# Performance work log

Hardware: AMD Instinct MI355X
Metric: run time of the kernel (lower is better)

The kernel has to match this reference:

```python
import jax, jax.numpy as jnp
import numpy as np

N = 50000          # num member nodes == num provider nodes
E = 800000         # provider->member bipartite edges (avg degree 16)
IN_M = 128; IN_P = 128; HID = 128; HEADS = 4; LAT = 64
NEG = 0.2          # leaky_relu negative slope (PyG GATConv default)


def gat_conv(x, src, dst, W, a_src, a_dst, b, heads, ch):
    """PyG-style GATConv (eval mode, concat heads). x:[N,F], src/dst:[Etot]."""
    n = x.shape[0]
    h = (x @ W).reshape(n, heads, ch)                       # [N,H,C]
    s = jnp.sum(h * a_src, axis=-1)                         # [N,H]
    d = jnp.sum(h * a_dst, axis=-1)                         # [N,H]
    e = jax.nn.leaky_relu(s[src] + d[dst], NEG)             # [Etot,H]
    # segment softmax over edges grouped by destination node
    m = jax.ops.segment_max(e, dst, num_segments=n)
    p = jnp.exp(e - m[dst])
    z = jax.ops.segment_sum(p, dst, num_segments=n)
    alpha = p / (z[dst] + 1e-16)                            # [Etot,H]
    out = jax.ops.segment_sum(h[src] * alpha[..., None], dst, num_segments=n)
    return out.reshape(n, heads * ch) + b


def setup_inputs() -> dict:
    key = jax.random.key(0)
    ks = jax.random.split(key, 24)
    gl = lambda k, shape, fan: (jax.random.normal(k, shape, jnp.float32) / np.sqrt(fan).astype(np.float32))
    return {
        "x_member": jax.random.normal(ks[0], (N, IN_M), jnp.float32),
        "x_provider": jax.random.normal(ks[1], (N, IN_P), jnp.float32),
        "edge_index": jax.random.randint(ks[2], (2, E), 0, N),
        "W1_m": gl(ks[3], (IN_M, HID), IN_M),
        "a_src1_m": gl(ks[4], (HEADS, HID // HEADS), HID // HEADS),
        "a_dst1_m": gl(ks[5], (HEADS, HID // HEADS), HID // HEADS),
        "b1_m": jnp.zeros((HID,), jnp.float32),
        "W2_m": gl(ks[6], (HID, LAT), HID),
        "a_src2_m": gl(ks[7], (1, LAT), LAT),
        "a_dst2_m": gl(ks[8], (1, LAT), LAT),
        "b2_m": jnp.zeros((LAT,), jnp.float32),
        "W1_p": gl(ks[9], (IN_P, HID), IN_P),
        "a_src1_p": gl(ks[10], (HEADS, HID // HEADS), HID // HEADS),
        "a_dst1_p": gl(ks[11], (HEADS, HID // HEADS), HID // HEADS),
        "b1_p": jnp.zeros((HID,), jnp.float32),
        "W2_p": gl(ks[12], (HID, LAT), HID),
        "a_src2_p": gl(ks[13], (1, LAT), LAT),
        "a_dst2_p": gl(ks[14], (1, LAT), LAT),
        "b2_p": jnp.zeros((LAT,), jnp.float32),
        "Wd_m": gl(ks[15], (LAT, IN_M), LAT),
        "bd_m": jnp.zeros((IN_M,), jnp.float32),
        "Wd_p": gl(ks[16], (LAT, IN_P), LAT),
        "bd_p": jnp.zeros((IN_P,), jnp.float32),
    }


def reference(x_member, x_provider, edge_index,
              W1_m, a_src1_m, a_dst1_m, b1_m, W2_m, a_src2_m, a_dst2_m, b2_m,
              W1_p, a_src1_p, a_dst1_p, b1_p, W2_p, a_src2_p, a_dst2_p, b2_p,
              Wd_m, bd_m, Wd_p, bd_p):
    prov, memb = edge_index[0], edge_index[1]
    loop = jnp.arange(N)
    # member graph: self loops + (provider -> member); provider graph: reverse
    m_src = jnp.concatenate([loop, prov]); m_dst = jnp.concatenate([loop, memb])
    p_src = jnp.concatenate([loop, memb]); p_dst = jnp.concatenate([loop, prov])

    xm = jax.nn.elu(gat_conv(x_member, m_src, m_dst, W1_m, a_src1_m, a_dst1_m, b1_m, HEADS, HID // HEADS))
    z_m = gat_conv(xm, m_src, m_dst, W2_m, a_src2_m, a_dst2_m, b2_m, 1, LAT)

    xp = jax.nn.elu(gat_conv(x_provider, p_src, p_dst, W1_p, a_src1_p, a_dst1_p, b1_p, HEADS, HID // HEADS))
    z_p = gat_conv(xp, p_src, p_dst, W2_p, a_src2_p, a_dst2_p, b2_p, 1, LAT)

    x_hat_member = z_m @ Wd_m + bd_m
    x_hat_provider = z_p @ Wd_p + bd_p
    edge_logits = jnp.sum(z_p[prov] * z_m[memb], axis=1)
    return (x_hat_member, x_hat_provider, edge_logits)
```

## Files before the change

### kernel.cpp

```cpp
#include <hip/hip_runtime.h>
#include <hip/hip_fp16.h>
#include <stdint.h>

__device__ __forceinline__ unsigned int pack_h2(float a, float b) {
    return (unsigned int)__half_as_ushort(__float2half(a)) |
           ((unsigned int)__half_as_ushort(__float2half(b)) << 16);
}
__device__ __forceinline__ float4 cvt_h4(uint2 r) {
    __half2 h0 = *reinterpret_cast<__half2*>(&r.x);
    __half2 h1 = *reinterpret_cast<__half2*>(&r.y);
    float2 f0 = __half22float2(h0), f1 = __half22float2(h1);
    return make_float4(f0.x, f0.y, f1.x, f1.y);
}

template<int K, int COUT, bool ADD_BIAS, bool IN_HALF, bool OUT_HALF, int SDH>
__global__ __launch_bounds__(256) void gemm_kernel(const void* __restrict__ X0,
                                                   const void* __restrict__ X1,
                                                   const float* __restrict__ W0,
                                                   const float* __restrict__ W1,
                                                   const float* __restrict__ b0,
                                                   const float* __restrict__ b1,
                                                   const float* __restrict__ as0,
                                                   const float* __restrict__ ad0,
                                                   const float* __restrict__ as1,
                                                   const float* __restrict__ ad1,
                                                   float* __restrict__ s_out,
                                                   float* __restrict__ d_out,
                                                   void* __restrict__ out0,
                                                   void* __restrict__ out1, int n)
{
    constexpr int KC   = 64;
    constexpr int CPT  = (COUT >= 128) ? 8 : 4;
    constexpr int TX   = COUT / CPT;
    constexpr int TY   = 256 / TX;
    constexpr int ROWS = TY * 4;

    __shared__ float Wl[KC * COUT];
    __shared__ float Xl[KC * ROWS];

    const int side = blockIdx.y;
    const void*  Xv   = side ? X1 : X0;
    const float* W    = side ? W1 : W0;
    const float* bias = side ? b1 : b0;
    void* outp        = side ? out1 : out0;

    const int tid  = threadIdx.x;
    const int row0 = blockIdx.x * ROWS;
    const int tx = tid % TX, ty = tid / TX;
    const int c0 = tx * CPT;

    float acc[4][CPT];
    #pragma unroll
    for (int i = 0; i < 4; ++i)
        #pragma unroll
        for (int j = 0; j < CPT; ++j) acc[i][j] = 0.f;

    for (int k0 = 0; k0 < K; k0 += KC) {
        for (int i = tid; i < KC * COUT / 4; i += 256) {
            int e0 = i * 4;
            int r = e0 / COUT, c = e0 - r * COUT;
            reinterpret_cast<float4*>(Wl)[i] =
                *reinterpret_cast<const float4*>(W + (size_t)(k0 + r) * COUT + c);
        }
        for (int i = tid; i < ROWS * KC / 4; i += 256) {
            int r = i / (KC / 4), c4 = i - r * (KC / 4);
            int gr = row0 + r;
            float4 v = make_float4(0.f, 0.f, 0.f, 0.f);
            if (gr < n) {
                if constexpr (IN_HALF) {
                    const __half* X = (const __half*)Xv;
                    v = cvt_h4(*reinterpret_cast<const uint2*>(X + (size_t)gr * K + k0 + c4 * 4));
                } else {
                    const float* X = (const float*)Xv;
                    v = *reinterpret_cast<const float4*>(X + (size_t)gr * K + k0 + c4 * 4);
                }
            }
            int cb = c4 * 4;
            Xl[(cb + 0) * ROWS + r] = v.x;
            Xl[(cb + 1) * ROWS + r] = v.y;
            Xl[(cb + 2) * ROWS + r] = v.z;
            Xl[(cb + 3) * ROWS + r] = v.w;
        }
        __syncthreads();

        #pragma unroll 16
        for (int kk = 0; kk < KC; ++kk) {
            float b[CPT];
            #pragma unroll
            for (int j = 0; j < CPT; ++j) b[j] = Wl[kk * COUT + c0 + j];
            float4 a4 = *reinterpret_cast<const float4*>(Xl + kk * ROWS + ty * 4);
            float a[4] = {a4.x, a4.y, a4.z, a4.w};
            #pragma unroll
            for (int i = 0; i < 4; ++i)
                #pragma unroll
                for (int j = 0; j < CPT; ++j)
                    acc[i][j] = fmaf(a[i], b[j], acc[i][j]);
        }
        __syncthreads();
    }

    float ascr[CPT], adtr[CPT];
    int hd = 0;
    if constexpr (SDH > 0) {
        constexpr int CHh = COUT / SDH;
        hd = c0 / CHh;
        const float* asc = (side ? as1 : as0) + c0;
        const float* adt = (side ? ad1 : ad0) + c0;
        #pragma unroll
        for (int j = 0; j < CPT; ++j) { ascr[j] = asc[j]; adtr[j] = adt[j]; }
    }

    #pragma unroll
    for (int i = 0; i < 4; ++i) {
        int gr = row0 + ty * 4 + i;
        if (gr < n) {
            float v[CPT];
            #pragma unroll
            for (int j = 0; j < CPT; ++j) {
                v[j] = acc[i][j];
                if constexpr (ADD_BIAS) v[j] += bias[c0 + j];
            }
            if constexpr (SDH > 0) {
                constexpr int CHh = COUT / SDH;
                constexpr int GL = CHh / CPT;
                float ps = 0.f, pd = 0.f;
                #pragma unroll
                for (int j = 0; j < CPT; ++j) {
                    ps = fmaf(v[j], ascr[j], ps);
                    pd = fmaf(v[j], adtr[j], pd);
                }
                #pragma unroll
                for (int o = 1; o < GL; o <<= 1) {
                    ps += __shfl_xor(ps, o, 64);
                    pd += __shfl_xor(pd, o, 64);
                }
                if ((tx % GL) == 0) {
                    size_t gi = (size_t)(side ? n + gr : gr) * SDH + hd;
                    s_out[gi] = ps; d_out[gi] = pd;
                }
            }
            if constexpr (OUT_HALF) {
                __half* po = (__half*)outp + (size_t)gr * COUT + c0;
                if constexpr (CPT == 8) {
                    uint4 w;
                    w.x = pack_h2(v[0], v[1]); w.y = pack_h2(v[2], v[3]);
                    w.z = pack_h2(v[4], v[5]); w.w = pack_h2(v[6], v[7]);
                    *reinterpret_cast<uint4*>(po) = w;
                } else {
                    uint2 w;
                    w.x = pack_h2(v[0], v[1]); w.y = pack_h2(v[2], v[3]);
                    *reinterpret_cast<uint2*>(po) = w;
                }
            } else {
                float* po = (float*)outp + (size_t)gr * COUT + c0;
                #pragma unroll
                for (int j = 0; j < CPT; ++j) po[j] = v[j];
            }
        }
    }
}

#define BSH 7
#define BCAP 2560
#define CHUNK_E 4096

__global__ __launch_bounds__(256) void bucket_scatter_kernel(const int* __restrict__ prov,
                                                             const int* __restrict__ memb,
                                                             int* __restrict__ bcnt,
                                                             int2* __restrict__ bstore,
                                                             int e, int n, int nbuck)
{
    __shared__ int hist[1024];
    __shared__ int lbase[1024];
    const int tid = threadIdx.x;
    const int e0 = blockIdx.x * CHUNK_E;
    const int e1 = min(e, e0 + CHUNK_E);

    for (int i = tid; i < nbuck; i += 256) hist[i] = 0;
    __syncthreads();
    for (int t = e0 + tid; t < e1; t += 256) {
        int m = memb[t], p = prov[t];
        atomicAdd(&hist[m >> BSH], 1);
        atomicAdd(&hist[(n + p) >> BSH], 1);
    }
    __syncthreads();
    for (int i = tid; i < nbuck; i += 256) {
        int h = hist[i];
        lbase[i] = (h > 0) ? atomicAdd(&bcnt[i], h) : 0;
        hist[i] = 0;
    }
    __syncthreads();
    for (int t = e0 + tid; t < e1; t += 256) {
        int m = memb[t], p = prov[t];
        int b1 = m >> BSH;
        int pos1 = lbase[b1] + atomicAdd(&hist[b1], 1);
        if (pos1 < BCAP) bstore[(size_t)b1 * BCAP + pos1] = make_int2(m, p);
        int d2 = n + p;
        int b2 = d2 >> BSH;
        int pos2 = lbase[b2] + atomicAdd(&hist[b2], 1);
        if (pos2 < BCAP) bstore[(size_t)b2 * BCAP + pos2] = make_int2(d2, m);
    }
}

__global__ __launch_bounds__(1024) void bucket_scan_kernel(const int* __restrict__ bcnt,
                                                           int* __restrict__ bbase,
                                                           int* __restrict__ roff,
                                                           int nb, int n2)
{
    __shared__ int tmp[1024];
    int tid = threadIdx.x;
    int v = (tid < nb) ? min(bcnt[tid], BCAP) : 0;
    tmp[tid] = v; __syncthreads();
    for (int o = 1; o < 1024; o <<= 1) {
        int x = (tid >= o) ? tmp[tid - o] : 0;
        __syncthreads();
        tmp[tid] += x;
        __syncthreads();
    }
    bbase[tid] = tmp[tid] - v;
    if (tid == 0) roff[n2] = tmp[1023];
}

__global__ __launch_bounds__(256) void bucket_build_kernel(const int* __restrict__ bcnt,
                                                           const int* __restrict__ bbase,
                                                           const int2* __restrict__ bstore,
                                                           int* __restrict__ roff,
                                                           int* __restrict__ colA,
                                                           int n2)
{
    __shared__ int2 ent[BCAP];
    __shared__ int  colL[BCAP];
    __shared__ int  cnts[128], pref[128], curs[128];

    const int b = blockIdx.x, tid = threadIdx.x;
    const int node0 = b << BSH;
    const int cnt  = min(bcnt[b], BCAP);
    const int base = bbase[b];

    if (tid < 128) cnts[tid] = 0;
    __syncthreads();
    for (int i = tid; i < cnt; i += 256) {
        int2 v = bstore[(size_t)b * BCAP + i];
        ent[i] = v;
        atomicAdd(&cnts[v.x - node0], 1);
    }
    __syncthreads();
    if (tid < 128) pref[tid] = cnts[tid];
    __syncthreads();
    #pragma unroll
    for (int o = 1; o < 128; o <<= 1) {
        int x = 0;
        if (tid < 128 && tid >= o) x = pref[tid - o];
        __syncthreads();
        if (tid < 128) pref[tid] += x;
        __syncthreads();
    }
    if (tid < 128) {
        int node = node0 + tid;
        if (node < n2) roff[node] = base + pref[tid] - cnts[tid];
        curs[tid] = 0;
    }
    __syncthreads();
    for (int i = tid; i < cnt; i += 256) {
        int2 v = ent[i];
        int loc = v.x - node0;
        int slot = (pref[loc] - cnts[loc]) + atomicAdd(&curs[loc], 1);
        colL[slot] = v.y;
    }
    __syncthreads();
    for (int i = tid; i < cnt; i += 256) colA[base + i] = colL[i];
}

template<int H>
__device__ __forceinline__ float selH(const float* arr, int hd) {
    float v = arr[0];
    #pragma unroll
    for (int hh = 1; hh < H; ++hh) v = (hd == hh) ? arr[hh] : v;
    return v;
}

template<int C, int H, bool ELU, bool OUTH>
__device__ __forceinline__ void agg_one_fullwave(int iG, int lN, int lane,
                                                 const __half* __restrict__ hf,
                                                 const float* __restrict__ sarr,
                                                 const float* __restrict__ sb,
                                                 const float* __restrict__ darr,
                                                 const int* __restrict__ roff,
                                                 const int* __restrict__ col,
                                                 const float* __restrict__ bias,
                                                 void* __restrict__ out,
                                                 float* alsW, int* srcsW)
{
    constexpr int CH = C / H;
    constexpr int LR = C / 4;
    constexpr int EP = 64 / LR;
    const int start = roff[iG], end = roff[iG + 1];
    const int deg = end - start;

    float dh[H], es[H];
    #pragma unroll
    for (int hh = 0; hh < H; ++hh) dh[hh] = darr[(size_t)iG * H + hh];
    #pragma unroll
    for (int hh = 0; hh < H; ++hh) {
        float e = sarr[(size_t)iG * H + hh] + dh[hh];
        es[hh] = fmaxf(e, 0.2f * e);
    }

    if (deg <= 64) {
        int srcL = (lane < deg) ? col[start + lane] : 0;
        float pl[H], zh[H];
        if (lane < deg) {
            #pragma unroll
            for (int hh = 0; hh < H; ++hh) {
                float e = sb[(size_t)srcL * H + hh] + dh[hh];
                pl[hh] = __expf(fmaxf(e, 0.2f * e));
            }
        } else {
            #pragma unroll
            for (int hh = 0; hh < H; ++hh) pl[hh] = 0.f;
        }
        #pragma unroll
        for (int hh = 0; hh < H; ++hh) zh[hh] = pl[hh];
        #pragma unroll
        for (int hh = 0; hh < H; ++hh)
            for (int o = 32; o >= 1; o >>= 1)
                zh[hh] += __shfl_xor(zh[hh], o, 64);
        if (lane < deg) srcsW[lane] = srcL;
        float aself[H];
        #pragma unroll
        for (int hh = 0; hh < H; ++hh) {
            float se = __expf(es[hh]);
            float invz = 1.f / (zh[hh] + se + 1e-16f);
            aself[hh] = se * invz;
            if (lane < deg) alsW[hh * 65 + lane] = pl[hh] * invz;
        }
        asm volatile("s_waitcnt lgkmcnt(0)" ::: "memory");

        const int sub = lane / LR;
        const int q   = lane % LR;
        const int c0  = q * 4;
        const int hd  = c0 / CH;

        float4 acc = make_float4(0.f, 0.f, 0.f, 0.f);
        if (sub == 0) {
            float4 hv = cvt_h4(*reinterpret_cast<const uint2*>(hf + (size_t)lN * C + c0));
            float a = selH<H>(aself, hd);
            acc.x = a * hv.x; acc.y = a * hv.y; acc.z = a * hv.z; acc.w = a * hv.w;
        }
        const float* alsB = alsW + hd * 65;
        int t = sub;
#define GSTEP(U)                                                                     \
        while (t + (U - 1) * EP < deg) {                                             \
            int ss[U]; float aa[U]; uint2 rr[U];                                     \
            _Pragma("unroll")                                                        \
            for (int u = 0; u < U; ++u) { ss[u] = srcsW[t + u * EP]; aa[u] = alsB[t + u * EP]; } \
            _Pragma("unroll")                                                        \
            for (int u = 0; u < U; ++u)                                              \
                rr[u] = *reinterpret_cast<const uint2*>(hf + (size_t)ss[u] * C + c0); \
            _Pragma("unroll")                                                        \
            for (int u = 0; u < U; ++u) {                                            \
                float4 hv = cvt_h4(rr[u]);                                           \
                acc.x = fmaf(aa[u], hv.x, acc.x);                                    \
                acc.y = fmaf(aa[u], hv.y, acc.y);                                    \
                acc.z = fmaf(aa[u], hv.z, acc.z);                                    \
                acc.w = fmaf(aa[u], hv.w, acc.w);                                    \
            }                                                                        \
            t += U * EP;                                                             \
        }
        GSTEP(8)
        GSTEP(4)
        GSTEP(2)
        GSTEP(1)
#undef GSTEP
        #pragma unroll
        for (int o = LR; o < 64; o <<= 1) {
            acc.x += __shfl_xor(acc.x, o, 64);
            acc.y += __shfl_xor(acc.y, o, 64);
            acc.z += __shfl_xor(acc.z, o, 64);
            acc.w += __shfl_xor(acc.w, o, 64);
        }
        if (sub == 0) {
            float4 bv = *reinterpret_cast<const float4*>(bias + c0);
            float4 v = make_float4(acc.x + bv.x, acc.y + bv.y, acc.z + bv.z, acc.w + bv.w);
            if constexpr (ELU) {
                v.x = (v.x > 0.f) ? v.x : (__expf(v.x) - 1.f);
                v.y = (v.y > 0.f) ? v.y : (__expf(v.y) - 1.f);
                v.z = (v.z > 0.f) ? v.z : (__expf(v.z) - 1.f);
                v.w = (v.w > 0.f) ? v.w : (__expf(v.w) - 1.f);
            }
            if constexpr (OUTH) {
                uint2 w; w.x = pack_h2(v.x, v.y); w.y = pack_h2(v.z, v.w);
                *reinterpret_cast<uint2*>((__half*)out + (size_t)lN * C + c0) = w;
            } else {
                *reinterpret_cast<float4*>((float*)out + (size_t)lN * C + c0) = v;
            }
        }
        return;
    }

    float zh[H];
    #pragma unroll
    for (int hh = 0; hh < H; ++hh) zh[hh] = 0.f;
    for (int base = start; base < end; base += 64) {
        int idx = base + lane;
        if (idx < end) {
            int src = col[idx];
            #pragma unroll
            for (int hh = 0; hh < H; ++hh) {
                float e = sb[(size_t)src * H + hh] + dh[hh];
                e = fmaxf(e, 0.2f * e);
                zh[hh] += __expf(e);
            }
        }
    }
    #pragma unroll
    for (int hh = 0; hh < H; ++hh) {
        for (int o = 32; o >= 1; o >>= 1) zh[hh] += __shfl_xor(zh[hh], o, 64);
        zh[hh] += __expf(es[hh]);
    }

    constexpr int CPL = C / 64;
    const int cc0 = lane * CPL;
    const int hdl = cc0 / CH;
    const float invz = 1.f / (zh[hdl] + 1e-16f);
    const float d_l  = dh[hdl];

    float acc2[CPL];
    {
        float aself = __expf(es[hdl]) * invz;
        #pragma unroll
        for (int j = 0; j < CPL; ++j) acc2[j] = aself * __half2float(hf[(size_t)lN * C + cc0 + j]);
    }
    for (int base = start; base < end; base += 64) {
        int idx = base + lane;
        int srcL2 = (idx < end) ? col[idx] : 0;
        int cnt2 = min(64, end - base);
        for (int t = 0; t < cnt2; ++t) {
            int st = __shfl(srcL2, t, 64);
            float e = sb[(size_t)st * H + hdl] + d_l;
            e = fmaxf(e, 0.2f * e);
            float a = __expf(e) * invz;
            #pragma unroll
            for (int j = 0; j < CPL; ++j)
                acc2[j] = fmaf(a, __half2float(hf[(size_t)st * C + cc0 + j]), acc2[j]);
        }
    }
    #pragma unroll
    for (int j = 0; j < CPL; ++j) {
        int c = cc0 + j;
        float v = acc2[j] + bias[c];
        if constexpr (ELU) v = (v > 0.f) ? v : (__expf(v) - 1.f);
        if constexpr (OUTH) ((__half*)out)[(size_t)lN * C + c] = __float2half(v);
        else                ((float*)out)[(size_t)lN * C + c] = v;
    }
}

template<int C, int H, bool ELU, bool OUTH>
__global__ __launch_bounds__(256) void agg_kernel(const __half* __restrict__ hm,
                                                  const __half* __restrict__ hp,
                                                  const float* __restrict__ sarr,
                                                  const float* __restrict__ darr,
                                                  const int* __restrict__ roff,
                                                  const int* __restrict__ col,
                                                  const float* __restrict__ bias_m,
                                                  const float* __restrict__ bias_p,
                                                  void* __restrict__ out_m,
                                                  void* __restrict__ out_p, int N)
{
    constexpr int CH  = C / H;
    constexpr int LRd = C / 8;
    constexpr int EPd = 32 / LRd;
    constexpr int H33 = H * 33;
    constexpr int ALSZ = (2 * H33 > H * 65) ? 2 * H33 : H * 65;
    __shared__ float als[4][ALSZ];
    __shared__ int   srcs[4][64];

    const int n2 = 2 * N;
    const int wslot = threadIdx.x >> 6;
    const int wv    = (blockIdx.x * 256 + threadIdx.x) >> 6;
    const int lane  = threadIdx.x & 63;
    const int g = lane >> 5, l = lane & 31;
    const int i0 = wv * 2;
    if (i0 >= n2) return;

    const bool nval = (i0 + g) < n2;
    const int iN = nval ? (i0 + g) : (n2 - 1);
    const int side = (iN >= N) ? 1 : 0;
    const int lN = iN - side * N;
    const __half* hf = side ? hp : hm;
    const float* sb = sarr + (size_t)side * N * H;
    const float* biasS = side ? bias_p : bias_m;
    void* outS = side ? out_p : out_m;

    const int start = roff[iN], end = roff[iN + 1];
    const int deg = nval ? (end - start) : 0;
    const int degO = __shfl_xor(deg, 32, 64);
    const int degm = max(deg, degO);

    if (degm <= 32) {
        float dh[H], es[H];
        if constexpr (H == 4) {
            float4 dv = *reinterpret_cast<const float4*>(darr + (size_t)iN * 4);
            float4 sv = *reinterpret_cast<const float4*>(sarr + (size_t)iN * 4);
            dh[0] = dv.x; dh[1] = dv.y; dh[2] = dv.z; dh[3] = dv.w;
            float ev[4] = {sv.x + dv.x, sv.y + dv.y, sv.z + dv.z, sv.w + dv.w};
            #pragma unroll
            for (int hh = 0; hh < 4; ++hh) es[hh] = fmaxf(ev[hh], 0.2f * ev[hh]);
        } else {
            #pragma unroll
            for (int hh = 0; hh < H; ++hh) {
                dh[hh] = darr[(size_t)iN * H + hh];
                float e = sarr[(size_t)iN * H + hh] + dh[hh];
                es[hh] = fmaxf(e, 0.2f * e);
            }
        }

        int srcL = (l < deg) ? col[start + l] : 0;
        float pl[H];
        if (l < deg) {
            if constexpr (H == 4) {
                float4 sv = *reinterpret_cast<const float4*>(sb + (size_t)srcL * 4);
                float ee[4] = {sv.x + dh[0], sv.y + dh[1], sv.z + dh[2], sv.w + dh[3]};
                #pragma unroll
                for (int hh = 0; hh < 4; ++hh) pl[hh] = __expf(fmaxf(ee[hh], 0.2f * ee[hh]));
            } else {
                #pragma unroll
                for (int hh = 0; hh < H; ++hh) {
                    float e = sb[(size_t)srcL * H + hh] + dh[hh];
                    pl[hh] = __expf(fmaxf(e, 0.2f * e));
                }
            }
        } else {
            #pragma unroll
            for (int hh = 0; hh < H; ++hh) pl[hh] = 0.f;
        }
        float zh[H];
        #pragma unroll
        for (int hh = 0; hh < H; ++hh) zh[hh] = pl[hh];
        #pragma unroll
        for (int hh = 0; hh < H; ++hh)
            #pragma unroll
            for (int o = 16; o >= 1; o >>= 1)
                zh[hh] += __shfl_xor(zh[hh], o, 64);
        if (l < deg) srcs[wslot][g * 32 + l] = srcL;
        float aself[H];
        #pragma unroll
        for (int hh = 0; hh < H; ++hh) {
            float se = __expf(es[hh]);
            float invz = 1.f / (zh[hh] + se + 1e-16f);
            aself[hh] = se * invz;
            if (l < deg) als[wslot][g * H33 + hh * 33 + l] = pl[hh] * invz;
        }
        asm volatile("s_waitcnt lgkmcnt(0)" ::: "memory");

        const int sub = l / LRd;
        const int q   = l % LRd;
        const int c0  = q * 8;
        const int hd  = c0 / CH;

        float acc[8];
        #pragma unroll
        for (int j = 0; j < 8; ++j) acc[j] = 0.f;
        if (sub == 0) {
            uint4 r = *reinterpret_cast<const uint4*>(hf + (size_t)lN * C + c0);
            float4 lo = cvt_h4(make_uint2(r.x, r.y));
            float4 hi = cvt_h4(make_uint2(r.z, r.w));
            float a = selH<H>(aself, hd);
            acc[0] = a * lo.x; acc[1] = a * lo.y; acc[2] = a * lo.z; acc[3] = a * lo.w;
            acc[4] = a * hi.x; acc[5] = a * hi.y; acc[6] = a * hi.z; acc[7] = a * hi.w;
        }
        const int*   srcB = &srcs[wslot][g * 32];
        const float* alsB = &als[wslot][g * H33 + hd * 33];
        int t = sub;
#define GSTEP(U)                                                                     \
        while (t + (U - 1) * EPd < deg) {                                            \
            int ss[U]; float aa[U]; uint4 rr[U];                                     \
            _Pragma("unroll")                                                        \
            for (int u = 0; u < U; ++u) { ss[u] = srcB[t + u * EPd]; aa[u] = alsB[t + u * EPd]; } \
            _Pragma("unroll")                                                        \
            for (int u = 0; u < U; ++u)                                              \
                rr[u] = *reinterpret_cast<const uint4*>(hf + (size_t)ss[u] * C + c0); \
            _Pragma("unroll")                                                        \
            for (int u = 0; u < U; ++u) {                                            \
                float4 lo = cvt_h4(make_uint2(rr[u].x, rr[u].y));                    \
                float4 hi = cvt_h4(make_uint2(rr[u].z, rr[u].w));                    \
                acc[0] = fmaf(aa[u], lo.x, acc[0]);                                  \
                acc[1] = fmaf(aa[u], lo.y, acc[1]);                                  \
                acc[2] = fmaf(aa[u], lo.z, acc[2]);                                  \
                acc[3] = fmaf(aa[u], lo.w, acc[3]);                                  \
                acc[4] = fmaf(aa[u], hi.x, acc[4]);                                  \
                acc[5] = fmaf(aa[u], hi.y, acc[5]);                                  \
                acc[6] = fmaf(aa[u], hi.z, acc[6]);                                  \
                acc[7] = fmaf(aa[u], hi.w, acc[7]);                                  \
            }                                                                        \
            t += U * EPd;                                                            \
        }
        GSTEP(8)
        GSTEP(4)
        GSTEP(2)
        GSTEP(1)
#undef GSTEP
        #pragma unroll
        for (int o = LRd; o < 32; o <<= 1) {
            #pragma unroll
            for (int j = 0; j < 8; ++j) acc[j] += __shfl_xor(acc[j], o, 64);
        }
        if (sub == 0 && nval) {
            float4 b0 = *reinterpret_cast<const float4*>(biasS + c0);
            float4 b1 = *reinterpret_cast<const float4*>(biasS + c0 + 4);
            float v[8] = {acc[0] + b0.x, acc[1] + b0.y, acc[2] + b0.z, acc[3] + b0.w,
                          acc[4] + b1.x, acc[5] + b1.y, acc[6] + b1.z, acc[7] + b1.w};
            if constexpr (ELU) {
                #pragma unroll
                for (int j = 0; j < 8; ++j) v[j] = (v[j] > 0.f) ? v[j] : (__expf(v[j]) - 1.f);
            }
            if constexpr (OUTH) {
                uint4 w;
                w.x = pack_h2(v[0], v[1]); w.y = pack_h2(v[2], v[3]);
                w.z = pack_h2(v[4], v[5]); w.w = pack_h2(v[6], v[7]);
                *reinterpret_cast<uint4*>((__half*)outS + (size_t)lN * C + c0) = w;
            } else {
                float* po = (float*)outS + (size_t)lN * C + c0;
                *reinterpret_cast<float4*>(po)     = make_float4(v[0], v[1], v[2], v[3]);
                *reinterpret_cast<float4*>(po + 4) = make_float4(v[4], v[5], v[6], v[7]);
            }
        }
        return;
    }

    for (int nd = 0; nd < 2; ++nd) {
        int i = i0 + nd;
        if (i >= n2) break;
        int sd2 = (i >= N) ? 1 : 0;
        int ln2 = i - sd2 * N;
        agg_one_fullwave<C, H, ELU, OUTH>(i, ln2, lane,
                                          sd2 ? hp : hm,
                                          sarr, sarr + (size_t)sd2 * N * H, darr,
                                          roff, col,
                                          sd2 ? bias_p : bias_m,
                                          sd2 ? out_p : out_m,
                                          als[wslot], srcs[wslot]);
    }
}

__global__ __launch_bounds__(256) void logits_kernel(const __half* __restrict__ zp,
                                                     const __half* __restrict__ zm,
                                                     const int* __restrict__ prov,
                                                     const int* __restrict__ memb,
                                                     float* __restrict__ outv, int e)
{
    const int nw   = (gridDim.x * 256) >> 6;
    const int wv   = (blockIdx.x * 256 + threadIdx.x) >> 6;
    const int lane = threadIdx.x & 63;
    const int g = lane >> 3, q = lane & 7;
    const int c0 = q * 8;
    for (int base = wv * 16; base < e; base += nw * 16) {
        int e1 = base + g, e2 = base + 8 + g;
        bool v1 = e1 < e, v2 = e2 < e;
        int i1 = v1 ? e1 : (e - 1), i2 = v2 ? e2 : (e - 1);
        int p1 = prov[i1], m1 = memb[i1];
        int p2 = prov[i2], m2 = memb[i2];
        uint4 a1 = *reinterpret_cast<const uint4*>(zp + (size_t)p1 * 64 + c0);
        uint4 b1 = *reinterpret_cast<const uint4*>(zm + (size_t)m1 * 64 + c0);
        uint4 a2 = *reinterpret_cast<const uint4*>(zp + (size_t)p2 * 64 + c0);
        uint4 b2 = *reinterpret_cast<const uint4*>(zm + (size_t)m2 * 64 + c0);
        float4 al1 = cvt_h4(make_uint2(a1.x, a1.y)), ah1 = cvt_h4(make_uint2(a1.z, a1.w));
        float4 bl1 = cvt_h4(make_uint2(b1.x, b1.y)), bh1 = cvt_h4(make_uint2(b1.z, b1.w));
        float4 al2 = cvt_h4(make_uint2(a2.x, a2.y)), ah2 = cvt_h4(make_uint2(a2.z, a2.w));
        float4 bl2 = cvt_h4(make_uint2(b2.x, b2.y)), bh2 = cvt_h4(make_uint2(b2.z, b2.w));
        float s1 = al1.x * bl1.x + al1.y * bl1.y + al1.z * bl1.z + al1.w * bl1.w
                 + ah1.x * bh1.x + ah1.y * bh1.y + ah1.z * bh1.z + ah1.w * bh1.w;
        float s2 = al2.x * bl2.x + al2.y * bl2.y + al2.z * bl2.z + al2.w * bl2.w
                 + ah2.x * bh2.x + ah2.y * bh2.y + ah2.z * bh2.z + ah2.w * bh2.w;
        #pragma unroll
        for (int o = 1; o < 8; o <<= 1) {
            s1 += __shfl_xor(s1, o, 64);
            s2 += __shfl_xor(s2, o, 64);
        }
        if (q == 0) {
            if (v1) outv[e1] = s1;
            if (v2) outv[e2] = s2;
        }
    }
}

extern "C" void kernel_launch(void* const* d_in, const int* in_sizes, int n_in,
                              void* d_out, int out_size, void* d_ws, size_t ws_size,
                              hipStream_t stream)
{
    const int N_ = in_sizes[0] / 128;
    const int E_ = in_sizes[2] / 2;

    const float* x_member   = (const float*)d_in[0];
    const float* x_provider = (const float*)d_in[1];
    const int*   prov = (const int*)d_in[2];
    const int*   memb = prov + E_;
    const float* W1_m = (const float*)d_in[3];
    const float* a_src1_m = (const float*)d_in[4];
    const float* a_dst1_m = (const float*)d_in[5];
    const float* b1_m = (const float*)d_in[6];
    const float* W2_m = (const float*)d_in[7];
    const float* a_src2_m = (const float*)d_in[8];
    const float* a_dst2_m = (const float*)d_in[9];
    const float* b2_m = (const float*)d_in[10];
    const float* W1_p = (const float*)d_in[11];
    const float* a_src1_p = (const float*)d_in[12];
    const float* a_dst1_p = (const float*)d_in[13];
    const float* b1_p = (const float*)d_in[14];
    const float* W2_p = (const float*)d_in[15];
    const float* a_src2_p = (const float*)d_in[16];
    const float* a_dst2_p = (const float*)d_in[17];
    const float* b2_p = (const float*)d_in[18];
    const float* Wd_m = (const float*)d_in[19];
    const float* bd_m = (const float*)d_in[20];
    const float* Wd_p = (const float*)d_in[21];
    const float* bd_p = (const float*)d_in[22];

    const int n2 = 2 * N_;
    const int NB = (n2 + 127) >> BSH;

    char* p = (char*)d_ws;
    auto alloc = [&](size_t bytes) { void* q = (void*)p; p += (bytes + 255) & ~(size_t)255; return q; };
    __half* h1m   = (__half*)alloc((size_t)N_ * 128 * 2);
    __half* h1p   = (__half*)alloc((size_t)N_ * 128 * 2);
    __half* xm16m = (__half*)alloc((size_t)N_ * 128 * 2);
    __half* xm16p = (__half*)alloc((size_t)N_ * 128 * 2);
    __half* zm16  = (__half*)alloc((size_t)N_ * 64 * 2);
    __half* zp16  = (__half*)alloc((size_t)N_ * 64 * 2);
    float* s1     = (float*)alloc((size_t)n2 * 4 * 4);
    float* d1     = (float*)alloc((size_t)n2 * 4 * 4);
    float* s2     = (float*)alloc((size_t)n2 * 4);
    float* d2     = (float*)alloc((size_t)n2 * 4);
    int*   bcnt   = (int*)alloc((size_t)NB * 4);
    int*   bbase  = (int*)alloc(1024 * 4);
    int*   roff2  = (int*)alloc((size_t)(n2 + 1) * 4);
    int*   colA   = (int*)alloc((size_t)2 * E_ * 4);
    __half* h2m = h1m;
    __half* h2p = h1p;
    int2*  bstore = (int2*)h1m;

    hipMemsetAsync(bcnt, 0, (size_t)NB * 4, stream);
    bucket_scatter_kernel<<<(E_ + CHUNK_E - 1) / CHUNK_E, 256, 0, stream>>>(prov, memb, bcnt, bstore, E_, N_, NB);
    bucket_scan_kernel<<<1, 1024, 0, stream>>>(bcnt, bbase, roff2, NB, n2);
    bucket_build_kernel<<<NB, 256, 0, stream>>>(bcnt, bbase, bstore, roff2, colA, n2);

    const dim3 gg((N_ + 63) / 64, 2);
    float* out = (float*)d_out;

    gemm_kernel<128, 128, false, false, true, 4><<<gg, 256, 0, stream>>>(
        x_member, x_provider, W1_m, W1_p, nullptr, nullptr,
        a_src1_m, a_dst1_m, a_src1_p, a_dst1_p, s1, d1, h1m, h1p, N_);
    agg_kernel<128, 4, true, true><<<(n2 + 7) / 8, 256, 0, stream>>>(
        h1m, h1p, s1, d1, roff2, colA, b1_m, b1_p, xm16m, xm16p, N_);

    gemm_kernel<128, 64, false, true, true, 1><<<gg, 256, 0, stream>>>(
        xm16m, xm16p, W2_m, W2_p, nullptr, nullptr,
        a_src2_m, a_dst2_m, a_src2_p, a_dst2_p, s2, d2, h2m, h2p, N_);
    agg_kernel<64, 1, false, true><<<(n2 + 7) / 8, 256, 0, stream>>>(
        h2m, h2p, s2, d2, roff2, colA, b2_m, b2_p, zm16, zp16, N_);

    gemm_kernel<64, 128, true, true, false, 0><<<gg, 256, 0, stream>>>(
        zm16, zp16, Wd_m, Wd_p, bd_m, bd_p,
        nullptr, nullptr, nullptr, nullptr, nullptr, nullptr,
        out, out + (size_t)N_ * 128, N_);
    logits_kernel<<<2048, 256, 0, stream>>>(zp16, zm16, prov, memb, out + (size_t)N_ * 128 * 2, E_);
}
```

Measured before the change: 483.1 us.

## Split GAT aggregation into separate attention-coefficient and feature-gather kernels

Each fused aggregation kernel is replaced by two kernels. An alpha kernel computes per-edge softmax coefficients and writes them as fp16 to global memory. A gather kernel then reads those coefficients and column indices straight from global memory and accumulates the neighbour features in a grid-stride loop over node pairs. The goal is to remove the LDS staging and the divergent high-degree path from the gather loop and to balance work across a fixed grid. In exchange it adds an extra kernel launch, extra global traffic for the alpha arrays, and fp16 rounding of the attention weights.

```diff
diff --git a/kernel.cpp b/kernel.cpp
--- a/kernel.cpp
+++ b/kernel.cpp
@@ -272,43 +272,39 @@
 }
 
 template<int H>
-__device__ __forceinline__ float selH(const float* arr, int hd) {
-    float v = arr[0];
-    #pragma unroll
-    for (int hh = 1; hh < H; ++hh) v = (hd == hh) ? arr[hh] : v;
-    return v;
-}
-
-template<int C, int H, bool ELU, bool OUTH>
-__device__ __forceinline__ void agg_one_fullwave(int iG, int lN, int lane,
-                                                 const __half* __restrict__ hf,
-                                                 const float* __restrict__ sarr,
-                                                 const float* __restrict__ sb,
-                                                 const float* __restrict__ darr,
-                                                 const int* __restrict__ roff,
-                                                 const int* __restrict__ col,
-                                                 const float* __restrict__ bias,
-                                                 void* __restrict__ out,
-                                                 float* alsW, int* srcsW)
-{
-    constexpr int CH = C / H;
-    constexpr int LR = C / 4;
-    constexpr int EP = 64 / LR;
+__device__ __forceinline__ void store_alpha(__half* __restrict__ A, size_t e, const float* a) {
+    if constexpr (H == 4) {
+        uint2 w; w.x = pack_h2(a[0], a[1]); w.y = pack_h2(a[2], a[3]);
+        *reinterpret_cast<uint2*>(A + e * 4) = w;
+    } else {
+        A[e] = __float2half(a[0]);
+    }
+}
+
+template<int H>
+__device__ __forceinline__ void alpha_one_fullwave(int iG, int lane,
+                                                   const float* __restrict__ sarr,
+                                                   const float* __restrict__ sb,
+                                                   const float* __restrict__ darr,
+                                                   const int* __restrict__ roff,
+                                                   const int* __restrict__ col,
+                                                   __half* __restrict__ A,
+                                                   __half* __restrict__ aselfA)
+{
     const int start = roff[iG], end = roff[iG + 1];
     const int deg = end - start;
 
     float dh[H], es[H];
     #pragma unroll
-    for (int hh = 0; hh < H; ++hh) dh[hh] = darr[(size_t)iG * H + hh];
-    #pragma unroll
     for (int hh = 0; hh < H; ++hh) {
+        dh[hh] = darr[(size_t)iG * H + hh];
         float e = sarr[(size_t)iG * H + hh] + dh[hh];
         es[hh] = fmaxf(e, 0.2f * e);
     }
 
     if (deg <= 64) {
         int srcL = (lane < deg) ? col[start + lane] : 0;
-        float pl[H], zh[H];
+        float pl[H];
         if (lane < deg) {
             #pragma unroll
             for (int hh = 0; hh < H; ++hh) {
@@ -319,82 +315,23 @@
             #pragma unroll
             for (int hh = 0; hh < H; ++hh) pl[hh] = 0.f;
         }
+        float zh[H];
         #pragma unroll
         for (int hh = 0; hh < H; ++hh) zh[hh] = pl[hh];
         #pragma unroll
         for (int hh = 0; hh < H; ++hh)
             for (int o = 32; o >= 1; o >>= 1)
                 zh[hh] += __shfl_xor(zh[hh], o, 64);
-        if (lane < deg) srcsW[lane] = srcL;
-        float aself[H];
+        float av[H], sf[H];
         #pragma unroll
         for (int hh = 0; hh < H; ++hh) {
             float se = __expf(es[hh]);
             float invz = 1.f / (zh[hh] + se + 1e-16f);
-            aself[hh] = se * invz;
-            if (lane < deg) alsW[hh * 65 + lane] = pl[hh] * invz;
-        }
-        asm volatile("s_waitcnt lgkmcnt(0)" ::: "memory");
-
-        const int sub = lane / LR;
-        const int q   = lane % LR;
-        const int c0  = q * 4;
-        const int hd  = c0 / CH;
-
-        float4 acc = make_float4(0.f, 0.f, 0.f, 0.f);
-        if (sub == 0) {
-            float4 hv = cvt_h4(*reinterpret_cast<const uint2*>(hf + (size_t)lN * C + c0));
-            float a = selH<H>(aself, hd);
-            acc.x = a * hv.x; acc.y = a * hv.y; acc.z = a * hv.z; acc.w = a * hv.w;
-        }
-        const float* alsB = alsW + hd * 65;
-        int t = sub;
-#define GSTEP(U)                                                                     \
-        while (t + (U - 1) * EP < deg) {                                             \
-            int ss[U]; float aa[U]; uint2 rr[U];                                     \
-            _Pragma("unroll")                                                        \
-            for (int u = 0; u < U; ++u) { ss[u] = srcsW[t + u * EP]; aa[u] = alsB[t + u * EP]; } \
-            _Pragma("unroll")                                                        \
-            for (int u = 0; u < U; ++u)                                              \
-                rr[u] = *reinterpret_cast<const uint2*>(hf + (size_t)ss[u] * C + c0); \
-            _Pragma("unroll")                                                        \
-            for (int u = 0; u < U; ++u) {                                            \
-                float4 hv = cvt_h4(rr[u]);                                           \
-                acc.x = fmaf(aa[u], hv.x, acc.x);                                    \
-                acc.y = fmaf(aa[u], hv.y, acc.y);                                    \
-                acc.z = fmaf(aa[u], hv.z, acc.z);                                    \
-                acc.w = fmaf(aa[u], hv.w, acc.w);                                    \
-            }                                                                        \
-            t += U * EP;                                                             \
-        }
-        GSTEP(8)
-        GSTEP(4)
-        GSTEP(2)
-        GSTEP(1)
-#undef GSTEP
-        #pragma unroll
-        for (int o = LR; o < 64; o <<= 1) {
-            acc.x += __shfl_xor(acc.x, o, 64);
-            acc.y += __shfl_xor(acc.y, o, 64);
-            acc.z += __shfl_xor(acc.z, o, 64);
-            acc.w += __shfl_xor(acc.w, o, 64);
-        }
-        if (sub == 0) {
-            float4 bv = *reinterpret_cast<const float4*>(bias + c0);
-            float4 v = make_float4(acc.x + bv.x, acc.y + bv.y, acc.z + bv.z, acc.w + bv.w);
-            if constexpr (ELU) {
-                v.x = (v.x > 0.f) ? v.x : (__expf(v.x) - 1.f);
-                v.y = (v.y > 0.f) ? v.y : (__expf(v.y) - 1.f);
-                v.z = (v.z > 0.f) ? v.z : (__expf(v.z) - 1.f);
-                v.w = (v.w > 0.f) ? v.w : (__expf(v.w) - 1.f);
-            }
-            if constexpr (OUTH) {
-                uint2 w; w.x = pack_h2(v.x, v.y); w.y = pack_h2(v.z, v.w);
-                *reinterpret_cast<uint2*>((__half*)out + (size_t)lN * C + c0) = w;
-            } else {
-                *reinterpret_cast<float4*>((float*)out + (size_t)lN * C + c0) = v;
-            }
-        }
+            sf[hh] = se * invz;
+            av[hh] = pl[hh] * invz;
+        }
+        if (lane < deg) store_alpha<H>(A, (size_t)(start + lane), av);
+        if (lane == 0) store_alpha<H>(aselfA, (size_t)iG, sf);
         return;
     }
 
@@ -414,149 +351,158 @@
         }
     }
     #pragma unroll
+    for (int hh = 0; hh < H; ++hh)
+        for (int o = 32; o >= 1; o >>= 1)
+            zh[hh] += __shfl_xor(zh[hh], o, 64);
+    float invz[H], sf[H];
+    #pragma unroll
     for (int hh = 0; hh < H; ++hh) {
-        for (int o = 32; o >= 1; o >>= 1) zh[hh] += __shfl_xor(zh[hh], o, 64);
-        zh[hh] += __expf(es[hh]);
-    }
-
-    constexpr int CPL = C / 64;
-    const int cc0 = lane * CPL;
-    const int hdl = cc0 / CH;
-    const float invz = 1.f / (zh[hdl] + 1e-16f);
-    const float d_l  = dh[hdl];
-
-    float acc2[CPL];
-    {
-        float aself = __expf(es[hdl]) * invz;
-        #pragma unroll
-        for (int j = 0; j < CPL; ++j) acc2[j] = aself * __half2float(hf[(size_t)lN * C + cc0 + j]);
-    }
+        float se = __expf(es[hh]);
+        invz[hh] = 1.f / (zh[hh] + se + 1e-16f);
+        sf[hh] = se * invz[hh];
+    }
+    if (lane == 0) store_alpha<H>(aselfA, (size_t)iG, sf);
     for (int base = start; base < end; base += 64) {
         int idx = base + lane;
-        int srcL2 = (idx < end) ? col[idx] : 0;
-        int cnt2 = min(64, end - base);
-        for (int t = 0; t < cnt2; ++t) {
-            int st = __shfl(srcL2, t, 64);
-            float e = sb[(size_t)st * H + hdl] + d_l;
-            e = fmaxf(e, 0.2f * e);
-            float a = __expf(e) * invz;
-            #pragma unroll
-            for (int j = 0; j < CPL; ++j)
-                acc2[j] = fmaf(a, __half2float(hf[(size_t)st * C + cc0 + j]), acc2[j]);
-        }
-    }
-    #pragma unroll
-    for (int j = 0; j < CPL; ++j) {
-        int c = cc0 + j;
-        float v = acc2[j] + bias[c];
-        if constexpr (ELU) v = (v > 0.f) ? v : (__expf(v) - 1.f);
-        if constexpr (OUTH) ((__half*)out)[(size_t)lN * C + c] = __float2half(v);
-        else                ((float*)out)[(size_t)lN * C + c] = v;
+        if (idx < end) {
+            int src = col[idx];
+            float av[H];
+            #pragma unroll
+            for (int hh = 0; hh < H; ++hh) {
+                float e = sb[(size_t)src * H + hh] + dh[hh];
+                e = fmaxf(e, 0.2f * e);
+                av[hh] = __expf(e) * invz[hh];
+            }
+            store_alpha<H>(A, (size_t)idx, av);
+        }
+    }
+}
+
+template<int H>
+__global__ __launch_bounds__(256) void alpha_kernel(const float* __restrict__ sarr,
+                                                    const float* __restrict__ darr,
+                                                    const int* __restrict__ roff,
+                                                    const int* __restrict__ col,
+                                                    __half* __restrict__ A,
+                                                    __half* __restrict__ aselfA, int N)
+{
+    const int n2 = 2 * N;
+    const int lane = threadIdx.x & 63;
+    const int g = lane >> 5, l = lane & 31;
+    const int nw  = (gridDim.x * 256) >> 6;
+    const int wv0 = (blockIdx.x * 256 + threadIdx.x) >> 6;
+    const int npair = (n2 + 1) >> 1;
+
+    for (int pr = wv0; pr < npair; pr += nw) {
+        const int i0 = pr * 2;
+        const bool nval = (i0 + g) < n2;
+        const int iN = nval ? (i0 + g) : (n2 - 1);
+        const int start = roff[iN], end = roff[iN + 1];
+        const int deg = nval ? (end - start) : 0;
+        const int degO = __shfl_xor(deg, 32, 64);
+
+        if (max(deg, degO) <= 32) {
+            const int side = (iN >= N) ? 1 : 0;
+            const float* sb = sarr + (size_t)side * N * H;
+            float dh[H], es[H];
+            if constexpr (H == 4) {
+                float4 dv = *reinterpret_cast<const float4*>(darr + (size_t)iN * 4);
+                float4 sv = *reinterpret_cast<const float4*>(sarr + (size_t)iN * 4);
+                dh[0] = dv.x; dh[1] = dv.y; dh[2] = dv.z; dh[3] = dv.w;
+                float ev[4] = {sv.x + dv.x, sv.y + dv.y, sv.z + dv.z, sv.w + dv.w};
+                #pragma unroll
+                for (int hh = 0; hh < 4; ++hh) es[hh] = fmaxf(ev[hh], 0.2f * ev[hh]);
+            } else {
+                #pragma unroll
+                for (int hh = 0; hh < H; ++hh) {
+                    dh[hh] = darr[(size_t)iN * H + hh];
+                    float e = sarr[(size_t)iN * H + hh] + dh[hh];
+                    es[hh] = fmaxf(e, 0.2f * e);
+                }
+            }
+            int srcL = (l < deg) ? col[start + l] : 0;
+            float pl[H];
+            if (l < deg) {
+                if constexpr (H == 4) {
+                    float4 sv = *reinterpret_cast<const float4*>(sb + (size_t)srcL * 4);
+                    float ee[4] = {sv.x + dh[0], sv.y + dh[1], sv.z + dh[2], sv.w + dh[3]};
+                    #pragma unroll
+                    for (int hh = 0; hh < 4; ++hh) pl[hh] = __expf(fmaxf(ee[hh], 0.2f * ee[hh]));
+                } else {
+                    #pragma unroll
+                    for (int hh = 0; hh < H; ++hh) {
+                        float e = sb[(size_t)srcL * H + hh] + dh[hh];
+                        pl[hh] = __expf(fmaxf(e, 0.2f * e));
+                    }
+                }
+            } else {
+                #pragma unroll
+                for (int hh = 0; hh < H; ++hh) pl[hh] = 0.f;
+            }
+            float zh[H];
+            #pragma unroll
+            for (int hh = 0; hh < H; ++hh) zh[hh] = pl[hh];
+            #pragma unroll
+            for (int hh = 0; hh < H; ++hh)
+                #pragma unroll
+                for (int o = 16; o >= 1; o >>= 1)
+                    zh[hh] += __shfl_xor(zh[hh], o, 64);
+            float av[H], sf[H];
+            #pragma unroll
+            for (int hh = 0; hh < H; ++hh) {
+                float se = __expf(es[hh]);
+                float invz = 1.f / (zh[hh] + se + 1e-16f);
+                sf[hh] = se * invz;
+                av[hh] = pl[hh] * invz;
+            }
+            if (l < deg) store_alpha<H>(A, (size_t)(start + l), av);
+            if (l == 0 && nval) store_alpha<H>(aselfA, (size_t)iN, sf);
+        } else {
+            for (int nd = 0; nd < 2; ++nd) {
+                int i = i0 + nd;
+                if (i >= n2) break;
+                int sd2 = (i >= N) ? 1 : 0;
+                alpha_one_fullwave<H>(i, lane, sarr, sarr + (size_t)sd2 * N * H, darr,
+                                      roff, col, A, aselfA);
+            }
+        }
     }
 }
 
 template<int C, int H, bool ELU, bool OUTH>
-__global__ __launch_bounds__(256) void agg_kernel(const __half* __restrict__ hm,
-                                                  const __half* __restrict__ hp,
-                                                  const float* __restrict__ sarr,
-                                                  const float* __restrict__ darr,
-                                                  const int* __restrict__ roff,
-                                                  const int* __restrict__ col,
-                                                  const float* __restrict__ bias_m,
-                                                  const float* __restrict__ bias_p,
-                                                  void* __restrict__ out_m,
-                                                  void* __restrict__ out_p, int N)
+__global__ __launch_bounds__(256) void gather_kernel(const __half* __restrict__ hm,
+                                                     const __half* __restrict__ hp,
+                                                     const __half* __restrict__ A,
+                                                     const __half* __restrict__ aselfA,
+                                                     const int* __restrict__ roff,
+                                                     const int* __restrict__ col,
+                                                     const float* __restrict__ bias_m,
+                                                     const float* __restrict__ bias_p,
+                                                     void* __restrict__ out_m,
+                                                     void* __restrict__ out_p, int N)
 {
     constexpr int CH  = C / H;
     constexpr int LRd = C / 8;
     constexpr int EPd = 32 / LRd;
-    constexpr int H33 = H * 33;
-    constexpr int ALSZ = (2 * H33 > H * 65) ? 2 * H33 : H * 65;
-    __shared__ float als[4][ALSZ];
-    __shared__ int   srcs[4][64];
-
     const int n2 = 2 * N;
-    const int wslot = threadIdx.x >> 6;
-    const int wv    = (blockIdx.x * 256 + threadIdx.x) >> 6;
-    const int lane  = threadIdx.x & 63;
+    const int lane = threadIdx.x & 63;
     const int g = lane >> 5, l = lane & 31;
-    const int i0 = wv * 2;
-    if (i0 >= n2) return;
-
-    const bool nval = (i0 + g) < n2;
-    const int iN = nval ? (i0 + g) : (n2 - 1);
-    const int side = (iN >= N) ? 1 : 0;
-    const int lN = iN - side * N;
-    const __half* hf = side ? hp : hm;
-    const float* sb = sarr + (size_t)side * N * H;
-    const float* biasS = side ? bias_p : bias_m;
-    void* outS = side ? out_p : out_m;
-
-    const int start = roff[iN], end = roff[iN + 1];
-    const int deg = nval ? (end - start) : 0;
-    const int degO = __shfl_xor(deg, 32, 64);
-    const int degm = max(deg, degO);
-
-    if (degm <= 32) {
-        float dh[H], es[H];
-        if constexpr (H == 4) {
-            float4 dv = *reinterpret_cast<const float4*>(darr + (size_t)iN * 4);
-            float4 sv = *reinterpret_cast<const float4*>(sarr + (size_t)iN * 4);
-            dh[0] = dv.x; dh[1] = dv.y; dh[2] = dv.z; dh[3] = dv.w;
-            float ev[4] = {sv.x + dv.x, sv.y + dv.y, sv.z + dv.z, sv.w + dv.w};
-            #pragma unroll
-            for (int hh = 0; hh < 4; ++hh) es[hh] = fmaxf(ev[hh], 0.2f * ev[hh]);
-        } else {
-            #pragma unroll
-            for (int hh = 0; hh < H; ++hh) {
-                dh[hh] = darr[(size_t)iN * H + hh];
-                float e = sarr[(size_t)iN * H + hh] + dh[hh];
-                es[hh] = fmaxf(e, 0.2f * e);
-            }
-        }
-
-        int srcL = (l < deg) ? col[start + l] : 0;
-        float pl[H];
-        if (l < deg) {
-            if constexpr (H == 4) {
-                float4 sv = *reinterpret_cast<const float4*>(sb + (size_t)srcL * 4);
-                float ee[4] = {sv.x + dh[0], sv.y + dh[1], sv.z + dh[2], sv.w + dh[3]};
-                #pragma unroll
-                for (int hh = 0; hh < 4; ++hh) pl[hh] = __expf(fmaxf(ee[hh], 0.2f * ee[hh]));
-            } else {
-                #pragma unroll
-                for (int hh = 0; hh < H; ++hh) {
-                    float e = sb[(size_t)srcL * H + hh] + dh[hh];
-                    pl[hh] = __expf(fmaxf(e, 0.2f * e));
-                }
-            }
-        } else {
-            #pragma unroll
-            for (int hh = 0; hh < H; ++hh) pl[hh] = 0.f;
-        }
-        float zh[H];
-        #pragma unroll
-        for (int hh = 0; hh < H; ++hh) zh[hh] = pl[hh];
-        #pragma unroll
-        for (int hh = 0; hh < H; ++hh)
-            #pragma unroll
-            for (int o = 16; o >= 1; o >>= 1)
-                zh[hh] += __shfl_xor(zh[hh], o, 64);
-        if (l < deg) srcs[wslot][g * 32 + l] = srcL;
-        float aself[H];
-        #pragma unroll
-        for (int hh = 0; hh < H; ++hh) {
-            float se = __expf(es[hh]);
-            float invz = 1.f / (zh[hh] + se + 1e-16f);
-            aself[hh] = se * invz;
-            if (l < deg) als[wslot][g * H33 + hh * 33 + l] = pl[hh] * invz;
-        }
-        asm volatile("s_waitcnt lgkmcnt(0)" ::: "memory");
-
-        const int sub = l / LRd;
-        const int q   = l % LRd;
-        const int c0  = q * 8;
-        const int hd  = c0 / CH;
+    const int sub = l / LRd, q = l % LRd;
+    const int c0 = q * 8;
+    const int hd = c0 / CH;
+    const int nw  = (gridDim.x * 256) >> 6;
+    const int wv0 = (blockIdx.x * 256 + threadIdx.x) >> 6;
+    const int npair = (n2 + 1) >> 1;
+
+    for (int pr = wv0; pr < npair; pr += nw) {
+        const int i0 = pr * 2;
+        const bool nval = (i0 + g) < n2;
+        const int iN = nval ? (i0 + g) : (n2 - 1);
+        const int side = (iN >= N) ? 1 : 0;
+        const int lN = iN - side * N;
+        const __half* hf = side ? hp : hm;
+        const int start = roff[iN];
+        const int deg = roff[iN + 1] - start;
 
         float acc[8];
         #pragma unroll
@@ -565,18 +511,20 @@
             uint4 r = *reinterpret_cast<const uint4*>(hf + (size_t)lN * C + c0);
             float4 lo = cvt_h4(make_uint2(r.x, r.y));
             float4 hi = cvt_h4(make_uint2(r.z, r.w));
-            float a = selH<H>(aself, hd);
+            float a = __half2float(aselfA[(size_t)iN * H + hd]);
             acc[0] = a * lo.x; acc[1] = a * lo.y; acc[2] = a * lo.z; acc[3] = a * lo.w;
             acc[4] = a * hi.x; acc[5] = a * hi.y; acc[6] = a * hi.z; acc[7] = a * hi.w;
         }
-        const int*   srcB = &srcs[wslot][g * 32];
-        const float* alsB = &als[wslot][g * H33 + hd * 33];
         int t = sub;
 #define GSTEP(U)                                                                     \
         while (t + (U - 1) * EPd < deg) {                                            \
             int ss[U]; float aa[U]; uint4 rr[U];                                     \
             _Pragma("unroll")                                                        \
-            for (int u = 0; u < U; ++u) { ss[u] = srcB[t + u * EPd]; aa[u] = alsB[t + u * EPd]; } \
+            for (int u = 0; u < U; ++u) {                                            \
+                int e = start + t + u * EPd;                                         \
+                ss[u] = col[e];                                                      \
+                aa[u] = __half2float(A[(size_t)e * H + hd]);                         \
+            }                                                                        \
             _Pragma("unroll")                                                        \
             for (int u = 0; u < U; ++u)                                              \
                 rr[u] = *reinterpret_cast<const uint4*>(hf + (size_t)ss[u] * C + c0); \
@@ -595,7 +543,6 @@
             }                                                                        \
             t += U * EPd;                                                            \
         }
-        GSTEP(8)
         GSTEP(4)
         GSTEP(2)
         GSTEP(1)
@@ -606,6 +553,7 @@
             for (int j = 0; j < 8; ++j) acc[j] += __shfl_xor(acc[j], o, 64);
         }
         if (sub == 0 && nval) {
+            const float* biasS = side ? bias_p : bias_m;
             float4 b0 = *reinterpret_cast<const float4*>(biasS + c0);
             float4 b1 = *reinterpret_cast<const float4*>(biasS + c0 + 4);
             float v[8] = {acc[0] + b0.x, acc[1] + b0.y, acc[2] + b0.z, acc[3] + b0.w,
@@ -615,31 +563,18 @@
                 for (int j = 0; j < 8; ++j) v[j] = (v[j] > 0.f) ? v[j] : (__expf(v[j]) - 1.f);
             }
             if constexpr (OUTH) {
+                __half* outS = (__half*)(side ? out_p : out_m);
                 uint4 w;
                 w.x = pack_h2(v[0], v[1]); w.y = pack_h2(v[2], v[3]);
                 w.z = pack_h2(v[4], v[5]); w.w = pack_h2(v[6], v[7]);
-                *reinterpret_cast<uint4*>((__half*)outS + (size_t)lN * C + c0) = w;
+                *reinterpret_cast<uint4*>(outS + (size_t)lN * C + c0) = w;
             } else {
-                float* po = (float*)outS + (size_t)lN * C + c0;
+                float* outS = (float*)(side ? out_p : out_m);
+                float* po = outS + (size_t)lN * C + c0;
                 *reinterpret_cast<float4*>(po)     = make_float4(v[0], v[1], v[2], v[3]);
                 *reinterpret_cast<float4*>(po + 4) = make_float4(v[4], v[5], v[6], v[7]);
             }
         }
-        return;
-    }
-
-    for (int nd = 0; nd < 2; ++nd) {
-        int i = i0 + nd;
-        if (i >= n2) break;
-        int sd2 = (i >= N) ? 1 : 0;
-        int ln2 = i - sd2 * N;
-        agg_one_fullwave<C, H, ELU, OUTH>(i, ln2, lane,
-                                          sd2 ? hp : hm,
-                                          sarr, sarr + (size_t)sd2 * N * H, darr,
-                                          roff, col,
-                                          sd2 ? bias_p : bias_m,
-                                          sd2 ? out_p : out_m,
-                                          als[wslot], srcs[wslot]);
     }
 }
 
@@ -729,8 +664,8 @@
     __half* zp16  = (__half*)alloc((size_t)N_ * 64 * 2);
     float* s1     = (float*)alloc((size_t)n2 * 4 * 4);
     float* d1     = (float*)alloc((size_t)n2 * 4 * 4);
-    float* s2     = (float*)alloc((size_t)n2 * 4);
-    float* d2     = (float*)alloc((size_t)n2 * 4);
+    __half* alpha2= (__half*)alloc((size_t)2 * E_ * 2);
+    __half* aselfH= (__half*)alloc((size_t)n2 * 4 * 2);
     int*   bcnt   = (int*)alloc((size_t)NB * 4);
     int*   bbase  = (int*)alloc(1024 * 4);
     int*   roff2  = (int*)alloc((size_t)(n2 + 1) * 4);
@@ -738,6 +673,7 @@
     __half* h2m = h1m;
     __half* h2p = h1p;
     int2*  bstore = (int2*)h1m;
+    __half* alpha1 = zm16;
 
     hipMemsetAsync(bcnt, 0, (size_t)NB * 4, stream);
     bucket_scatter_kernel<<<(E_ + CHUNK_E - 1) / CHUNK_E, 256, 0, stream>>>(prov, memb, bcnt, bstore, E_, N_, NB);
@@ -750,14 +686,16 @@
     gemm_kernel<128, 128, false, false, true, 4><<<gg, 256, 0, stream>>>(
         x_member, x_provider, W1_m, W1_p, nullptr, nullptr,
         a_src1_m, a_dst1_m, a_src1_p, a_dst1_p, s1, d1, h1m, h1p, N_);
-    agg_kernel<128, 4, true, true><<<(n2 + 7) / 8, 256, 0, stream>>>(
-        h1m, h1p, s1, d1, roff2, colA, b1_m, b1_p, xm16m, xm16p, N_);
+    alpha_kernel<4><<<2048, 256, 0, stream>>>(s1, d1, roff2, colA, alpha1, aselfH, N_);
+    gather_kernel<128, 4, true, true><<<2048, 256, 0, stream>>>(
+        h1m, h1p, alpha1, aselfH, roff2, colA, b1_m, b1_p, xm16m, xm16p, N_);
 
     gemm_kernel<128, 64, false, true, true, 1><<<gg, 256, 0, stream>>>(
         xm16m, xm16p, W2_m, W2_p, nullptr, nullptr,
-        a_src2_m, a_dst2_m, a_src2_p, a_dst2_p, s2, d2, h2m, h2p, N_);
-    agg_kernel<64, 1, false, true><<<(n2 + 7) / 8, 256, 0, stream>>>(
-        h2m, h2p, s2, d2, roff2, colA, b2_m, b2_p, zm16, zp16, N_);
+        a_src2_m, a_dst2_m, a_src2_p, a_dst2_p, s1, d1, h2m, h2p, N_);
+    alpha_kernel<1><<<2048, 256, 0, stream>>>(s1, d1, roff2, colA, alpha2, aselfH, N_);
+    gather_kernel<64, 1, false, true><<<2048, 256, 0, stream>>>(
+        h2m, h2p, alpha2, aselfH, roff2, colA, b2_m, b2_p, zm16, zp16, N_);
 
     gemm_kernel<64, 128, true, true, false, 0><<<gg, 256, 0, stream>>>(
         zm16, zp16, Wd_m, Wd_p, bd_m, bd_p,
```

After: 474.3 us. No clear change (-1.8%).
